# Kernel optimization log

Measured on AMD Instinct MI355X. Metric: run time of the kernel, lower is better.

The kernel has to match this reference:

```python
import jax, jax.numpy as jnp
import numpy as np
from jax import lax

K = 9  # 3x3 kernel points


def _gather(feat, iy, ix):
    """feat: [B,C,H,W]; iy,ix: [B,K,H,W] int32. Zero padding outside bounds.
    Returns [B,C,K,H,W]."""
    B, C, H, W = feat.shape
    valid = ((iy >= 0) & (iy < H) & (ix >= 0) & (ix < W))
    iyc = jnp.clip(iy, 0, H - 1)
    ixc = jnp.clip(ix, 0, W - 1)
    flat = (iyc * W + ixc).reshape(B, 1, -1)            # [B,1,K*H*W]
    g = jnp.take_along_axis(feat.reshape(B, C, H * W), flat, axis=2)
    g = g.reshape(B, C, K, H, W)
    return g * valid[:, None].astype(feat.dtype)


def _bilinear(feat, ys, xs):
    """feat: [B,C,H,W]; ys,xs: [B,K,H,W] float sampling coords -> [B,C,K,H,W]."""
    y0 = jnp.floor(ys)
    x0 = jnp.floor(xs)
    wy = (ys - y0)[:, None]
    wx = (xs - x0)[:, None]
    y0i = y0.astype(jnp.int32)
    x0i = x0.astype(jnp.int32)
    y1i = y0i + 1
    x1i = x0i + 1
    v00 = _gather(feat, y0i, x0i)
    v01 = _gather(feat, y0i, x1i)
    v10 = _gather(feat, y1i, x0i)
    v11 = _gather(feat, y1i, x1i)
    return (v00 * (1 - wy) * (1 - wx) + v01 * (1 - wy) * wx
            + v10 * wy * (1 - wx) + v11 * wy * wx)


def _deform_layer(x, w_off, b_off, w, b, dilation=1):
    """Modulated deformable 3x3 conv, stride 1, padding=dilation (same size)."""
    B, C, H, W = x.shape
    # offset/mask conv (regular 3x3 conv, same padding)
    om = lax.conv_general_dilated(
        x, w_off, window_strides=(1, 1),
        padding=[(dilation, dilation), (dilation, dilation)],
        rhs_dilation=(dilation, dilation),
        dimension_numbers=('NCHW', 'OIHW', 'NCHW')) + b_off[None, :, None, None]
    off = om[:, :2 * K].reshape(B, K, 2, H, W)   # (dy, dx) per kernel point
    mask = jax.nn.sigmoid(om[:, 2 * K:])         # [B,K,H,W]
    dy = off[:, :, 0]
    dx = off[:, :, 1]
    # base kernel grid offsets (-d, 0, +d)
    ky, kx = jnp.meshgrid(jnp.arange(3), jnp.arange(3), indexing='ij')
    base_y = ((ky.reshape(-1) - 1) * dilation).astype(x.dtype)   # [K]
    base_x = ((kx.reshape(-1) - 1) * dilation).astype(x.dtype)
    gy = jnp.arange(H, dtype=x.dtype)
    gx = jnp.arange(W, dtype=x.dtype)
    ys = gy[None, None, :, None] + base_y[None, :, None, None] + dy  # [B,K,H,W]
    xs = gx[None, None, None, :] + base_x[None, :, None, None] + dx
    sampled = _bilinear(x, ys, xs) * mask[:, None]   # [B,C,K,H,W]
    wk = w.reshape(w.shape[0], w.shape[1], K)        # [O,I,K]
    out = jnp.einsum('bikhw,oik->bohw', sampled, wk) + b[None, :, None, None]
    return out


def setup_inputs() -> dict:
    key = jax.random.key(0)
    ks = jax.random.split(key, 16)
    B, C, H, W = 4, 256, 64, 64
    O = 256
    inp = {'x': jax.random.normal(ks[0], (B, C, H, W), jnp.float32)}
    chans = [(C, C), (C, O), (O, O)]  # layer i==num_layers-2 maps in->out
    for i, (ci, co) in enumerate(chans):
        k = jax.random.split(ks[i + 1], 4)
        # offset conv: 27 = 3*K channels (18 offsets + 9 masks); small init
        inp[f'w_off{i}'] = jax.random.normal(k[0], (3 * K, ci, 3, 3), jnp.float32) * 0.01
        inp[f'b_off{i}'] = jnp.zeros((3 * K,), jnp.float32)
        # deform conv weight: kaiming normal, fan_in = ci*K
        std = np.sqrt(2.0 / (ci * K)).astype(np.float32)
        inp[f'w{i}'] = jax.random.normal(k[1], (co, ci, 3, 3), jnp.float32) * std
        inp[f'b{i}'] = jnp.zeros((co,), jnp.float32)
    return inp


def reference(x, w_off0, b_off0, w0, b0, w_off1, b_off1, w1, b1,
              w_off2, b_off2, w2, b2):
    params = [(w_off0, b_off0, w0, b0),
              (w_off1, b_off1, w1, b1),
              (w_off2, b_off2, w2, b2)]
    for (wo, bo, w, b) in params:
        x = jax.nn.relu(_deform_layer(x, wo, bo, w, b, dilation=1))
    return x
```

## Files before the change

### kernel.cpp

```cpp
#include <hip/hip_runtime.h>
#include <math.h>

#define Bn 4
#define Cn 256
#define Hn 64
#define Wn 64
#define On 256
#define HWn 4096
#define Pn 16384
#define Kc 2304

#define LGKM0 0xc07f

typedef _Float16 half8 __attribute__((ext_vector_type(8)));
typedef float floatx4 __attribute__((ext_vector_type(4)));

__global__ void k_init(const float* __restrict__ x, _Float16* __restrict__ act0,
                       const float* __restrict__ w0, const float* __restrict__ w1,
                       const float* __restrict__ w2, const float* __restrict__ wo0,
                       const float* __restrict__ wo1, const float* __restrict__ wo2,
                       _Float16* __restrict__ wtp, _Float16* __restrict__ wbop) {
  int bx = blockIdx.x;
  int tid = threadIdx.x;
  if (bx < 1024) {
    __shared__ float Tf[64][65];
    int b = bx >> 8;
    int c0 = ((bx >> 6) & 3) << 6;
    int hw0 = (bx & 63) << 6;
    const float* ib = x + ((size_t)b * Cn + c0) * HWn + hw0;
    _Float16* ob = act0 + ((size_t)b * HWn + hw0) * Cn + c0;
    int ty = tid >> 4, tx = tid & 15;
#pragma unroll
    for (int p = 0; p < 4; ++p) {
      int ch = p * 16 + ty;
      float4 v = *(const float4*)(ib + (size_t)ch * HWn + tx * 4);
      Tf[ch][tx * 4 + 0] = v.x;
      Tf[ch][tx * 4 + 1] = v.y;
      Tf[ch][tx * 4 + 2] = v.z;
      Tf[ch][tx * 4 + 3] = v.w;
    }
    __syncthreads();
    int hwR = tid >> 3, seg = tid & 7;
#pragma unroll
    for (int p = 0; p < 2; ++p) {
      int hw = p * 32 + hwR;
      half8 h;
#pragma unroll
      for (int k = 0; k < 8; ++k) h[k] = (_Float16)Tf[seg * 8 + k][hw];
      *(half8*)(ob + (size_t)hw * Cn + seg * 8) = h;
    }
  } else if (bx < 1792) {
    int b2 = bx - 1024;
    int l = b2 >> 8;
    int n = b2 & 255;
    const float* w = (l == 0) ? w0 : (l == 1) ? w1 : w2;
    _Float16* dst = wtp + (size_t)l * 256 * Kc;
    int g = n >> 4, col = n & 15;
#pragma unroll
    for (int e2 = tid; e2 < 288; e2 += 256) {
      int c = e2 >> 3;
      int r = e2 & 7;
      int kq = r >> 2;
      int quad = r & 3;
      int t = c >> 2;
      int cq = c & 3;
      const float* s = w + (size_t)n * 2304 + (size_t)(cq * 64 + kq * 32 + quad * 8) * 9 + t;
      half8 h;
#pragma unroll
      for (int e = 0; e < 8; ++e) h[e] = (_Float16)s[e * 9];
      *(half8*)(dst + ((size_t)((c * 16 + g) * 2 + kq)) * 512 + (quad * 16 + col) * 8) = h;
    }
  } else {
    int b3 = bx - 1792;
    int l = b3 >> 5;
    int n = b3 & 31;
    const float* w = (l == 0) ? wo0 : (l == 1) ? wo1 : wo2;
    _Float16* dst = wbop + (size_t)l * 36 * 2048;
    int g = n >> 4, col = n & 15;
#pragma unroll
    for (int e2 = tid; e2 < 288; e2 += 256) {
      int c = e2 >> 3;
      int r = e2 & 7;
      int kq = r >> 2;
      int quad = r & 3;
      int cw = c / 9;
      int t = c - cw * 9;
      half8 h;
      if (n < 27) {
        const float* s = w + ((size_t)n * 256 + cw * 64 + kq * 32 + quad * 8) * 9 + t;
#pragma unroll
        for (int e = 0; e < 8; ++e) h[e] = (_Float16)s[e * 9];
      } else {
#pragma unroll
        for (int e = 0; e < 8; ++e) h[e] = (_Float16)0.f;
      }
      *(half8*)(dst + ((size_t)((c * 2 + g) * 2 + kq)) * 512 + (quad * 16 + col) * 8) = h;
    }
  }
}

__global__ __launch_bounds__(512) void k_layer(
    const _Float16* __restrict__ xh,
    const _Float16* __restrict__ wbop, const float* __restrict__ boff,
    const _Float16* __restrict__ wtp, const float* __restrict__ bias,
    _Float16* __restrict__ outh, float* __restrict__ outf) {
  __shared__ __align__(16) _Float16 As[2][64][72];
  __shared__ __align__(16) _Float16 Bs[2][16384];
  __shared__ __align__(16) _Float16 win[3 * 66 * 64];
  __shared__ __align__(16) float omS[64 * 33];
  __shared__ __align__(16) float sampS[64][9][8];

  int bid = blockIdx.x;
  int lb = ((bid & 7) << 5) + (bid >> 3);
  int p0 = lb * 64;
  int tid = threadIdx.x;
  int lane = tid & 63;
  int wave = tid >> 6;
  int quad = lane >> 4;
  int col = lane & 15;

  int ar = tid >> 3;
  int aci = (tid & 7) * 8;

  int yB = (p0 & 4095) >> 6;
  int bB = p0 >> 12;

  half8 zero8;
#pragma unroll
  for (int e = 0; e < 8; ++e) zero8[e] = (_Float16)0.f;

  int mi = wave >> 1;
  int ng = wave & 1;

  floatx4 acc1 = (floatx4){0.f, 0.f, 0.f, 0.f};
  half8 boA[2], boB[2];
#pragma unroll
  for (int kq = 0; kq < 2; ++kq) {
    boA[kq] = *(const half8*)(wbop + (size_t)(ng * 2 + kq) * 512 + lane * 8);
    boB[kq] = *(const half8*)(wbop + 2048 + (size_t)(ng * 2 + kq) * 512 + lane * 8);
  }

#pragma unroll 1
  for (int cg = 0; cg < 4; ++cg) {
    for (int e = tid; e < 1584; e += 512) {
      int seg = e & 7;
      int rowpx = e >> 3;
      int r = rowpx / 66;
      int px = rowpx - r * 66;
      int yy = yB + r - 1;
      int xx = px - 1;
      half8 v = zero8;
      if (((unsigned)yy < 64u) & ((unsigned)xx < 64u))
        v = *(const half8*)(xh + ((size_t)((bB * Hn + yy) * Wn + xx)) * Cn +
                            cg * 64 + seg * 8);
      int ba = (rowpx * 128 + seg * 16) ^ ((px & 7) << 4);
      *(half8*)((char*)win + ba) = v;
    }
    __syncthreads();

#pragma unroll
    for (int t = 0; t < 9; ++t) {
      int cp = cg * 9 + t;
      int dty = t / 3;
      int dtx = t % 3;
#pragma unroll
      for (int kq = 0; kq < 2; ++kq) {
        int pxw = mi * 16 + col + dtx;
        int ba = ((dty * 66 + pxw) * 128 + kq * 64 + quad * 16) ^ ((pxw & 7) << 4);
        half8 af = *(const half8*)((const char*)win + ba);
        acc1 = __builtin_amdgcn_mfma_f32_16x16x32_f16(
            af, (cp & 1) ? boB[kq] : boA[kq], acc1, 0, 0, 0);
      }
      if (cp + 2 < 36) {
        const _Float16* wob = wbop + (size_t)(cp + 2) * 2048;
#pragma unroll
        for (int kq = 0; kq < 2; ++kq) {
          half8 v2 = *(const half8*)(wob + (size_t)(ng * 2 + kq) * 512 + lane * 8);
          if (cp & 1) boB[kq] = v2; else boA[kq] = v2;
        }
      }
    }
    __syncthreads();
  }

  {
    int n1 = ng * 16 + col;
    if (n1 < 27) {
      float bb = boff[n1];
#pragma unroll
      for (int r = 0; r < 4; ++r)
        omS[(mi * 16 + quad * 4 + r) * 33 + n1] = acc1[r] + bb;
    }
  }
  __syncthreads();

  for (int e = tid; e < 576; e += 512) {
    int lp = e / 9;
    int k = e - lp * 9;
    int pp = p0 + lp;
    int bi = pp >> 12;
    int pyx = pp & 4095;
    int py = pyx >> 6, px = pyx & 63;

    float dy = omS[lp * 33 + 2 * k];
    float dx = omS[lp * 33 + 2 * k + 1];
    float m = 1.f / (1.f + expf(-omS[lp * 33 + 18 + k]));

    float ys = (float)(py + k / 3 - 1) + dy;
    float xs = (float)(px + k % 3 - 1) + dx;
    float y0f = floorf(ys), x0f = floorf(xs);
    float wy = ys - y0f, wx = xs - x0f;
    int y0 = (int)y0f, x0 = (int)x0f;
    int y1 = y0 + 1, x1 = x0 + 1;

    bool vy0 = (y0 >= 0) & (y0 < Hn);
    bool vy1 = (y1 >= 0) & (y1 < Hn);
    bool vx0 = (x0 >= 0) & (x0 < Wn);
    bool vx1 = (x1 >= 0) & (x1 < Wn);
    int y0c = min(max(y0, 0), Hn - 1), y1c = min(max(y1, 0), Hn - 1);
    int x0c = min(max(x0, 0), Wn - 1), x1c = min(max(x1, 0), Wn - 1);

    int base = bi * HWn;
    float* s = &sampS[lp][k][0];
    ((int*)s)[0] = (base + y0c * Wn + x0c) * Cn;
    ((int*)s)[1] = (base + y0c * Wn + x1c) * Cn;
    ((int*)s)[2] = (base + y1c * Wn + x0c) * Cn;
    ((int*)s)[3] = (base + y1c * Wn + x1c) * Cn;
    s[4] = (vy0 && vx0) ? m * (1.f - wy) * (1.f - wx) : 0.f;
    s[5] = (vy0 && vx1) ? m * (1.f - wy) * wx : 0.f;
    s[6] = (vy1 && vx0) ? m * wy * (1.f - wx) : 0.f;
    s[7] = (vy1 && vx1) ? m * wy * wx : 0.f;
  }
  __syncthreads();

  int mw = wave >> 2;
  int nw = wave & 3;

  float bj[4];
#pragma unroll
  for (int j = 0; j < 4; ++j) bj[j] = bias[(nw * 4 + j) * 16 + col];

  floatx4 acc[2][4];
#pragma unroll
  for (int i = 0; i < 2; ++i)
#pragma unroll
    for (int j = 0; j < 4; ++j) acc[i][j] = (floatx4){0.f, 0.f, 0.f, 0.f};

  half8 g00, g01, g10, g11;
  half8 bst0[4], bst1[4];
  int4 ofsC, ofsN;
  float4 wvC, wvN;

  ofsC = *(const int4*)&sampS[ar][0][0];
  wvC = *(const float4*)&sampS[ar][0][4];
  ofsN = ofsC; wvN = wvC;
  g00 = *(const half8*)(xh + (size_t)ofsC.x + aci);
  g01 = *(const half8*)(xh + (size_t)ofsC.y + aci);
  g10 = *(const half8*)(xh + (size_t)ofsC.z + aci);
  g11 = *(const half8*)(xh + (size_t)ofsC.w + aci);
#pragma unroll
  for (int q = 0; q < 4; ++q)
    bst0[q] = *(const half8*)(wtp + (size_t)(q * 512 + tid) * 8);
#pragma unroll
  for (int q = 0; q < 4; ++q)
    bst1[q] = *(const half8*)(wtp + 16384 + (size_t)(q * 512 + tid) * 8);

#pragma unroll 1
  for (int t = 0; t < 9; ++t) {
    if (t < 8) {
      ofsN = *(const int4*)&sampS[ar][t + 1][0];
      wvN = *(const float4*)&sampS[ar][t + 1][4];
    }
#pragma unroll
    for (int cc = 0; cc < 4; ++cc) {
      {
        _Float16 h00 = (_Float16)wvC.x, h01 = (_Float16)wvC.y;
        _Float16 h10 = (_Float16)wvC.z, h11 = (_Float16)wvC.w;
        half8 r;
#pragma unroll
        for (int e = 0; e < 8; ++e)
          r[e] = g00[e] * h00 + g01[e] * h01 + g10[e] * h10 + g11[e] * h11;
        *(half8*)&As[cc & 1][ar][aci] = r;
      }
#pragma unroll
      for (int q = 0; q < 4; ++q)
        *(half8*)&Bs[cc & 1][(q * 512 + tid) * 8] = (cc & 1) ? bst1[q] : bst0[q];
      if (cc < 3) {
        int ci = (cc + 1) * 64 + aci;
        g00 = *(const half8*)(xh + (size_t)ofsC.x + ci);
        g01 = *(const half8*)(xh + (size_t)ofsC.y + ci);
        g10 = *(const half8*)(xh + (size_t)ofsC.z + ci);
        g11 = *(const half8*)(xh + (size_t)ofsC.w + ci);
      } else if (t < 8) {
        g00 = *(const half8*)(xh + (size_t)ofsN.x + aci);
        g01 = *(const half8*)(xh + (size_t)ofsN.y + aci);
        g10 = *(const half8*)(xh + (size_t)ofsN.z + aci);
        g11 = *(const half8*)(xh + (size_t)ofsN.w + aci);
      }
      if (cc < 2 || t < 8) {
        const _Float16* wsrc = wtp + ((size_t)(4 * t) + cc + 2) * 16384;
#pragma unroll
        for (int q = 0; q < 4; ++q) {
          half8 v = *(const half8*)(wsrc + (size_t)(q * 512 + tid) * 8);
          if (cc & 1) bst1[q] = v; else bst0[q] = v;
        }
      }

      __builtin_amdgcn_s_waitcnt(LGKM0);
      __builtin_amdgcn_s_barrier();

      half8 af[2][2];
#pragma unroll
      for (int kq = 0; kq < 2; ++kq)
#pragma unroll
        for (int i = 0; i < 2; ++i)
          af[kq][i] =
              *(const half8*)&As[cc & 1][mw * 32 + i * 16 + col][kq * 32 + quad * 8];

      half8 bf[2][4];
#pragma unroll
      for (int kq = 0; kq < 2; ++kq)
#pragma unroll
        for (int j = 0; j < 4; ++j)
          bf[kq][j] =
              *(const half8*)&Bs[cc & 1][((nw * 4 + j) * 2 + kq) * 512 + lane * 8];

#pragma unroll
      for (int kq = 0; kq < 2; ++kq)
#pragma unroll
        for (int i = 0; i < 2; ++i)
#pragma unroll
          for (int j = 0; j < 4; ++j)
            acc[i][j] = __builtin_amdgcn_mfma_f32_16x16x32_f16(
                af[kq][i], bf[kq][j], acc[i][j], 0, 0, 0);
    }
    ofsC = ofsN;
    wvC = wvN;
  }

#pragma unroll
  for (int i = 0; i < 2; ++i)
#pragma unroll
    for (int j = 0; j < 4; ++j) {
      int n = (nw * 4 + j) * 16 + col;
      if (outf) {
        int pb = p0 + mw * 32 + i * 16 + quad * 4;
        int bi = pb >> 12;
        int pyx = pb & 4095;
        float4 v;
        v.x = fmaxf(acc[i][j][0] + bj[j], 0.f);
        v.y = fmaxf(acc[i][j][1] + bj[j], 0.f);
        v.z = fmaxf(acc[i][j][2] + bj[j], 0.f);
        v.w = fmaxf(acc[i][j][3] + bj[j], 0.f);
        *(float4*)(outf + ((size_t)(bi * On + n)) * HWn + pyx) = v;
      } else {
#pragma unroll
        for (int r = 0; r < 4; ++r) {
          int pp = p0 + mw * 32 + i * 16 + quad * 4 + r;
          float v = fmaxf(acc[i][j][r] + bj[j], 0.f);
          outh[(size_t)pp * On + n] = (_Float16)v;
        }
      }
    }
}

extern "C" void kernel_launch(void* const* d_in, const int* in_sizes, int n_in,
                              void* d_out, int out_size, void* d_ws, size_t ws_size,
                              hipStream_t stream) {
  (void)in_sizes; (void)n_in; (void)out_size; (void)ws_size;
  const float* x = (const float*)d_in[0];

  _Float16* act0h = (_Float16*)d_ws;
  _Float16* act1h = act0h + (size_t)Pn * Cn;
  _Float16* wbop  = act1h + (size_t)Pn * Cn;
  _Float16* wtp   = wbop + (size_t)3 * 36 * 2048;

  k_init<<<1888, 256, 0, stream>>>(
      x, act0h,
      (const float*)d_in[3], (const float*)d_in[7], (const float*)d_in[11],
      (const float*)d_in[1], (const float*)d_in[5], (const float*)d_in[9],
      wtp, wbop);

  _Float16* cur = act0h;
  _Float16* nxt = act1h;
  for (int l = 0; l < 3; ++l) {
    const float* b_off = (const float*)d_in[2 + l * 4];
    const float* b     = (const float*)d_in[4 + l * 4];
    k_layer<<<Pn / 64, 512, 0, stream>>>(
        cur, wbop + (size_t)l * 36 * 2048, b_off,
        wtp + (size_t)l * 256 * Kc, b, nxt,
        (l == 2) ? (float*)d_out : nullptr);
    _Float16* tswap = cur; cur = nxt; nxt = tswap;
  }
}
```

Before: 231.7 us.

## Halve pixel tile, drop LDS weight staging, load MFMA B operands from global

The layer kernel now processes 32 pixels per block instead of 64 and launches twice as many blocks, with launch bounds raised to allow more resident blocks. The shared-memory B (weight) buffer is removed, so each wave loads its own weight fragments straight from global memory into registers, and the weight prefetch moves after the MFMAs. The aim is to cut LDS use and the cost of writing and reading the weight tile so occupancy rises. In exchange, only half the threads build the gathered A tile, the offset-conv stage uses only four waves, and weights are re-read from global/L2 by twice as many blocks.

```diff
diff --git a/kernel.cpp b/kernel.cpp
--- a/kernel.cpp
+++ b/kernel.cpp
@@ -99,56 +99,60 @@
   }
 }
 
-__global__ __launch_bounds__(512) void k_layer(
+__global__ __launch_bounds__(512, 4) void k_layer(
     const _Float16* __restrict__ xh,
     const _Float16* __restrict__ wbop, const float* __restrict__ boff,
     const _Float16* __restrict__ wtp, const float* __restrict__ bias,
     _Float16* __restrict__ outh, float* __restrict__ outf) {
-  __shared__ __align__(16) _Float16 As[2][64][72];
-  __shared__ __align__(16) _Float16 Bs[2][16384];
-  __shared__ __align__(16) _Float16 win[3 * 66 * 64];
-  __shared__ __align__(16) float omS[64 * 33];
-  __shared__ __align__(16) float sampS[64][9][8];
+  __shared__ __align__(16) _Float16 As[2][32][72];
+  __shared__ __align__(16) _Float16 win[3 * 34 * 64];
+  __shared__ __align__(16) float omS[32 * 33];
+  __shared__ __align__(16) float sampS[32][9][8];
 
   int bid = blockIdx.x;
-  int lb = ((bid & 7) << 5) + (bid >> 3);
-  int p0 = lb * 64;
+  int lb = ((bid & 7) << 6) + (bid >> 3);
+  int p0 = lb * 32;
   int tid = threadIdx.x;
   int lane = tid & 63;
   int wave = tid >> 6;
   int quad = lane >> 4;
   int col = lane & 15;
 
-  int ar = tid >> 3;
+  bool gth = tid < 256;
+  int ar = (tid & 255) >> 3;
   int aci = (tid & 7) * 8;
 
   int yB = (p0 & 4095) >> 6;
   int bB = p0 >> 12;
+  int x0B = p0 & 63;
 
   half8 zero8;
 #pragma unroll
   for (int e = 0; e < 8; ++e) zero8[e] = (_Float16)0.f;
 
-  int mi = wave >> 1;
+  int mi = (wave >> 1) & 1;
   int ng = wave & 1;
+  bool p1c = wave < 4;
 
   floatx4 acc1 = (floatx4){0.f, 0.f, 0.f, 0.f};
   half8 boA[2], boB[2];
-#pragma unroll
-  for (int kq = 0; kq < 2; ++kq) {
-    boA[kq] = *(const half8*)(wbop + (size_t)(ng * 2 + kq) * 512 + lane * 8);
-    boB[kq] = *(const half8*)(wbop + 2048 + (size_t)(ng * 2 + kq) * 512 + lane * 8);
+  if (p1c) {
+#pragma unroll
+    for (int kq = 0; kq < 2; ++kq) {
+      boA[kq] = *(const half8*)(wbop + (size_t)(ng * 2 + kq) * 512 + lane * 8);
+      boB[kq] = *(const half8*)(wbop + 2048 + (size_t)(ng * 2 + kq) * 512 + lane * 8);
+    }
   }
 
 #pragma unroll 1
   for (int cg = 0; cg < 4; ++cg) {
-    for (int e = tid; e < 1584; e += 512) {
+    for (int e = tid; e < 816; e += 512) {
       int seg = e & 7;
       int rowpx = e >> 3;
-      int r = rowpx / 66;
-      int px = rowpx - r * 66;
+      int r = rowpx / 34;
+      int px = rowpx - r * 34;
       int yy = yB + r - 1;
-      int xx = px - 1;
+      int xx = x0B + px - 1;
       half8 v = zero8;
       if (((unsigned)yy < 64u) & ((unsigned)xx < 64u))
         v = *(const half8*)(xh + ((size_t)((bB * Hn + yy) * Wn + xx)) * Cn +
@@ -161,29 +165,31 @@
 #pragma unroll
     for (int t = 0; t < 9; ++t) {
       int cp = cg * 9 + t;
-      int dty = t / 3;
-      int dtx = t % 3;
-#pragma unroll
-      for (int kq = 0; kq < 2; ++kq) {
-        int pxw = mi * 16 + col + dtx;
-        int ba = ((dty * 66 + pxw) * 128 + kq * 64 + quad * 16) ^ ((pxw & 7) << 4);
-        half8 af = *(const half8*)((const char*)win + ba);
-        acc1 = __builtin_amdgcn_mfma_f32_16x16x32_f16(
-            af, (cp & 1) ? boB[kq] : boA[kq], acc1, 0, 0, 0);
-      }
-      if (cp + 2 < 36) {
-        const _Float16* wob = wbop + (size_t)(cp + 2) * 2048;
+      if (p1c) {
+        int dty = t / 3;
+        int dtx = t % 3;
 #pragma unroll
         for (int kq = 0; kq < 2; ++kq) {
-          half8 v2 = *(const half8*)(wob + (size_t)(ng * 2 + kq) * 512 + lane * 8);
-          if (cp & 1) boB[kq] = v2; else boA[kq] = v2;
+          int pxw = mi * 16 + col + dtx;
+          int ba = ((dty * 34 + pxw) * 128 + kq * 64 + quad * 16) ^ ((pxw & 7) << 4);
+          half8 af = *(const half8*)((const char*)win + ba);
+          acc1 = __builtin_amdgcn_mfma_f32_16x16x32_f16(
+              af, (cp & 1) ? boB[kq] : boA[kq], acc1, 0, 0, 0);
         }
+        if (cp + 2 < 36) {
+          const _Float16* wob = wbop + (size_t)(cp + 2) * 2048;
+#pragma unroll
+          for (int kq = 0; kq < 2; ++kq) {
+            half8 v2 = *(const half8*)(wob + (size_t)(ng * 2 + kq) * 512 + lane * 8);
+            if (cp & 1) boB[kq] = v2; else boA[kq] = v2;
+          }
+        }
       }
     }
     __syncthreads();
   }
 
-  {
+  if (p1c) {
     int n1 = ng * 16 + col;
     if (n1 < 27) {
       float bb = boff[n1];
@@ -194,7 +200,8 @@
   }
   __syncthreads();
 
-  for (int e = tid; e < 576; e += 512) {
+  if (tid < 288) {
+    int e = tid;
     int lp = e / 9;
     int k = e - lp * 9;
     int pp = p0 + lp;
@@ -233,47 +240,49 @@
   }
   __syncthreads();
 
-  int mw = wave >> 2;
-  int nw = wave & 3;
-
-  float bj[4];
-#pragma unroll
-  for (int j = 0; j < 4; ++j) bj[j] = bias[(nw * 4 + j) * 16 + col];
-
-  floatx4 acc[2][4];
+  float bj[2];
+#pragma unroll
+  for (int j = 0; j < 2; ++j) bj[j] = bias[(wave * 2 + j) * 16 + col];
+
+  floatx4 acc[2][2];
 #pragma unroll
   for (int i = 0; i < 2; ++i)
 #pragma unroll
-    for (int j = 0; j < 4; ++j) acc[i][j] = (floatx4){0.f, 0.f, 0.f, 0.f};
+    for (int j = 0; j < 2; ++j) acc[i][j] = (floatx4){0.f, 0.f, 0.f, 0.f};
 
   half8 g00, g01, g10, g11;
-  half8 bst0[4], bst1[4];
-  int4 ofsC, ofsN;
-  float4 wvC, wvN;
-
-  ofsC = *(const int4*)&sampS[ar][0][0];
-  wvC = *(const float4*)&sampS[ar][0][4];
-  ofsN = ofsC; wvN = wvC;
-  g00 = *(const half8*)(xh + (size_t)ofsC.x + aci);
-  g01 = *(const half8*)(xh + (size_t)ofsC.y + aci);
-  g10 = *(const half8*)(xh + (size_t)ofsC.z + aci);
-  g11 = *(const half8*)(xh + (size_t)ofsC.w + aci);
-#pragma unroll
-  for (int q = 0; q < 4; ++q)
-    bst0[q] = *(const half8*)(wtp + (size_t)(q * 512 + tid) * 8);
-#pragma unroll
-  for (int q = 0; q < 4; ++q)
-    bst1[q] = *(const half8*)(wtp + 16384 + (size_t)(q * 512 + tid) * 8);
+  half8 bwA[2][2], bwB[2][2];
+  int4 ofsC = {0, 0, 0, 0}, ofsN = {0, 0, 0, 0};
+  float4 wvC = {0.f, 0.f, 0.f, 0.f}, wvN = wvC;
+
+  if (gth) {
+    ofsC = *(const int4*)&sampS[ar][0][0];
+    wvC = *(const float4*)&sampS[ar][0][4];
+    ofsN = ofsC; wvN = wvC;
+    g00 = *(const half8*)(xh + (size_t)ofsC.x + aci);
+    g01 = *(const half8*)(xh + (size_t)ofsC.y + aci);
+    g10 = *(const half8*)(xh + (size_t)ofsC.z + aci);
+    g11 = *(const half8*)(xh + (size_t)ofsC.w + aci);
+  }
+#pragma unroll
+  for (int kq = 0; kq < 2; ++kq)
+#pragma unroll
+    for (int j = 0; j < 2; ++j) {
+      bwA[kq][j] = *(const half8*)(wtp +
+          (size_t)((wave * 2 + j) * 2 + kq) * 512 + lane * 8);
+      bwB[kq][j] = *(const half8*)(wtp + 16384 +
+          (size_t)((wave * 2 + j) * 2 + kq) * 512 + lane * 8);
+    }
 
 #pragma unroll 1
   for (int t = 0; t < 9; ++t) {
-    if (t < 8) {
+    if (gth && t < 8) {
       ofsN = *(const int4*)&sampS[ar][t + 1][0];
       wvN = *(const float4*)&sampS[ar][t + 1][4];
     }
 #pragma unroll
     for (int cc = 0; cc < 4; ++cc) {
-      {
+      if (gth) {
         _Float16 h00 = (_Float16)wvC.x, h01 = (_Float16)wvC.y;
         _Float16 h10 = (_Float16)wvC.z, h11 = (_Float16)wvC.w;
         half8 r;
@@ -281,58 +290,51 @@
         for (int e = 0; e < 8; ++e)
           r[e] = g00[e] * h00 + g01[e] * h01 + g10[e] * h10 + g11[e] * h11;
         *(half8*)&As[cc & 1][ar][aci] = r;
-      }
-#pragma unroll
-      for (int q = 0; q < 4; ++q)
-        *(half8*)&Bs[cc & 1][(q * 512 + tid) * 8] = (cc & 1) ? bst1[q] : bst0[q];
-      if (cc < 3) {
-        int ci = (cc + 1) * 64 + aci;
-        g00 = *(const half8*)(xh + (size_t)ofsC.x + ci);
-        g01 = *(const half8*)(xh + (size_t)ofsC.y + ci);
-        g10 = *(const half8*)(xh + (size_t)ofsC.z + ci);
-        g11 = *(const half8*)(xh + (size_t)ofsC.w + ci);
-      } else if (t < 8) {
-        g00 = *(const half8*)(xh + (size_t)ofsN.x + aci);
-        g01 = *(const half8*)(xh + (size_t)ofsN.y + aci);
-        g10 = *(const half8*)(xh + (size_t)ofsN.z + aci);
-        g11 = *(const half8*)(xh + (size_t)ofsN.w + aci);
-      }
+        if (cc < 3) {
+          int ci = (cc + 1) * 64 + aci;
+          g00 = *(const half8*)(xh + (size_t)ofsC.x + ci);
+          g01 = *(const half8*)(xh + (size_t)ofsC.y + ci);
+          g10 = *(const half8*)(xh + (size_t)ofsC.z + ci);
+          g11 = *(const half8*)(xh + (size_t)ofsC.w + ci);
+        } else if (t < 8) {
+          g00 = *(const half8*)(xh + (size_t)ofsN.x + aci);
+          g01 = *(const half8*)(xh + (size_t)ofsN.y + aci);
+          g10 = *(const half8*)(xh + (size_t)ofsN.z + aci);
+          g11 = *(const half8*)(xh + (size_t)ofsN.w + aci);
+        }
+      }
+
+      __builtin_amdgcn_s_waitcnt(LGKM0);
+      __builtin_amdgcn_s_barrier();
+
+      half8 af[2][2];
+#pragma unroll
+      for (int kq = 0; kq < 2; ++kq)
+#pragma unroll
+        for (int i = 0; i < 2; ++i)
+          af[kq][i] =
+              *(const half8*)&As[cc & 1][i * 16 + col][kq * 32 + quad * 8];
+
+#pragma unroll
+      for (int kq = 0; kq < 2; ++kq)
+#pragma unroll
+        for (int i = 0; i < 2; ++i)
+#pragma unroll
+          for (int j = 0; j < 2; ++j)
+            acc[i][j] = __builtin_amdgcn_mfma_f32_16x16x32_f16(
+                af[kq][i], (cc & 1) ? bwB[kq][j] : bwA[kq][j], acc[i][j], 0, 0, 0);
+
       if (cc < 2 || t < 8) {
         const _Float16* wsrc = wtp + ((size_t)(4 * t) + cc + 2) * 16384;
 #pragma unroll
-        for (int q = 0; q < 4; ++q) {
-          half8 v = *(const half8*)(wsrc + (size_t)(q * 512 + tid) * 8);
-          if (cc & 1) bst1[q] = v; else bst0[q] = v;
-        }
-      }
-
-      __builtin_amdgcn_s_waitcnt(LGKM0);
-      __builtin_amdgcn_s_barrier();
-
-      half8 af[2][2];
-#pragma unroll
-      for (int kq = 0; kq < 2; ++kq)
-#pragma unroll
-        for (int i = 0; i < 2; ++i)
-          af[kq][i] =
-              *(const half8*)&As[cc & 1][mw * 32 + i * 16 + col][kq * 32 + quad * 8];
-
-      half8 bf[2][4];
-#pragma unroll
-      for (int kq = 0; kq < 2; ++kq)
-#pragma unroll
-        for (int j = 0; j < 4; ++j)
-          bf[kq][j] =
-              *(const half8*)&Bs[cc & 1][((nw * 4 + j) * 2 + kq) * 512 + lane * 8];
-
-#pragma unroll
-      for (int kq = 0; kq < 2; ++kq)
-#pragma unroll
-        for (int i = 0; i < 2; ++i)
-#pragma unroll
-          for (int j = 0; j < 4; ++j)
-            acc[i][j] = __builtin_amdgcn_mfma_f32_16x16x32_f16(
-                af[kq][i], bf[kq][j], acc[i][j], 0, 0, 0);
+        for (int kq = 0; kq < 2; ++kq)
+#pragma unroll
+          for (int j = 0; j < 2; ++j) {
+            half8 v = *(const half8*)(wsrc +
+                (size_t)((wave * 2 + j) * 2 + kq) * 512 + lane * 8);
+            if (cc & 1) bwB[kq][j] = v; else bwA[kq][j] = v;
+          }
+      }
     }
     ofsC = ofsN;
     wvC = wvN;
@@ -341,10 +343,10 @@
 #pragma unroll
   for (int i = 0; i < 2; ++i)
 #pragma unroll
-    for (int j = 0; j < 4; ++j) {
-      int n = (nw * 4 + j) * 16 + col;
+    for (int j = 0; j < 2; ++j) {
+      int n = (wave * 2 + j) * 16 + col;
       if (outf) {
-        int pb = p0 + mw * 32 + i * 16 + quad * 4;
+        int pb = p0 + i * 16 + quad * 4;
         int bi = pb >> 12;
         int pyx = pb & 4095;
         float4 v;
@@ -356,7 +358,7 @@
       } else {
 #pragma unroll
         for (int r = 0; r < 4; ++r) {
-          int pp = p0 + mw * 32 + i * 16 + quad * 4 + r;
+          int pp = p0 + i * 16 + quad * 4 + r;
           float v = fmaxf(acc[i][j][r] + bj[j], 0.f);
           outh[(size_t)pp * On + n] = (_Float16)v;
         }
@@ -386,7 +388,7 @@
   for (int l = 0; l < 3; ++l) {
     const float* b_off = (const float*)d_in[2 + l * 4];
     const float* b     = (const float*)d_in[4 + l * 4];
-    k_layer<<<Pn / 64, 512, 0, stream>>>(
+    k_layer<<<Pn / 32, 512, 0, stream>>>(
         cur, wbop + (size_t)l * 36 * 2048, b_off,
         wtp + (size_t)l * 256 * Kc, b, nxt,
         (l == 2) ? (float*)d_out : nullptr);
```

New measurement: 245.3 us. 1.06x slower.
